# Kernel tuning notes

Measured on AMD Instinct MI355X. Metric: run time of the kernel, lower is better.

The kernel has to match this reference:

```python
import jax, jax.numpy as jnp
import numpy as np
import math

C_Z, C_HID, N_HEADS = 128, 32, 4
B, N = 1, 320
LN_EPS = 1e-5


def setup_inputs() -> dict:
    key = jax.random.key(0)
    ks = jax.random.split(key, 9)
    d = C_HID * N_HEADS  # 128
    glorot = math.sqrt(2.0 / (C_Z + d))
    return {
        "z": jax.random.normal(ks[0], (B, N, N, C_Z), jnp.float32),
        "mask_bias": jax.random.normal(ks[1], (B, N, 1, 1, N), jnp.float32),
        "edge_bias": jax.random.normal(ks[2], (B, 1, N_HEADS, N, N), jnp.float32),
        "wq": jax.random.normal(ks[3], (d, C_Z), jnp.float32) * glorot,
        "wk": jax.random.normal(ks[4], (d, C_Z), jnp.float32) * glorot,
        "wv": jax.random.normal(ks[5], (d, C_Z), jnp.float32) * glorot,
        "wg": jax.random.normal(ks[6], (d, C_Z), jnp.float32) * 0.02,
        "wo": jax.random.normal(ks[7], (C_Z, d), jnp.float32) * 0.02,
        "ln_w": jnp.ones((C_Z,), jnp.float32),
        "ln_b": jnp.zeros((C_Z,), jnp.float32),
    }


def reference(z, mask_bias, edge_bias, wq, wk, wv, wg, wo, ln_w, ln_b):
    # LayerNorm over c_z
    mu = jnp.mean(z, axis=-1, keepdims=True)
    var = jnp.mean(jnp.square(z - mu), axis=-1, keepdims=True)
    zn = (z - mu) * jax.lax.rsqrt(var + LN_EPS) * ln_w + ln_b  # [B,I,J,c_z]

    def proj(w):
        p = jnp.einsum("bijd,ed->bije", zn, w)  # [B,I,J,H*c]
        p = p.reshape(zn.shape[:-1] + (N_HEADS, C_HID))  # [B,I,J,H,c]
        return jnp.swapaxes(p, -3, -2)  # [B,I,H,J,c]

    q = proj(wq) / math.sqrt(C_HID)
    k = proj(wk)
    v = proj(wv)

    # scores: [B,I,H,Q,K] + mask_bias [B,I,1,1,K] + edge_bias [B,1,H,Q,K]
    scores = jnp.einsum("bihqc,bihkc->bihqk", q, k) + mask_bias + edge_bias
    a = jax.nn.softmax(scores, axis=-1)
    o = jnp.einsum("bihqk,bihkc->bihqc", a, v)  # [B,I,H,J,c]
    o = jnp.swapaxes(o, -3, -2)  # [B,I,J,H,c]

    g = jax.nn.sigmoid(jnp.einsum("bijd,ed->bije", zn, wg))
    g = g.reshape(zn.shape[:-1] + (N_HEADS, C_HID))
    o = o * g

    o = o.reshape(o.shape[:-2] + (N_HEADS * C_HID,))  # [B,I,J,H*c]
    return jnp.einsum("bije,de->bijd", o, wo)  # [B,I,J,c_z]
```

## Files before the change

### kernel.cpp

```cpp
#include <hip/hip_runtime.h>
#include <hip/hip_bf16.h>

#define NRES 320
#define CZ 128
#define NH 4
#define CH 32
#define DM 128
#define NPOS (NRES*NRES)
#define LN_EPS 1e-5f
#define QSCALE 0.17677669529663687f
#define LOG2E 1.4426950408889634f

using bf16 = __hip_bfloat16;
typedef __attribute__((ext_vector_type(8))) short short8;
typedef __attribute__((ext_vector_type(4))) float floatx4;

__device__ __forceinline__ float bflo(uint32_t u){ return __uint_as_float(u << 16); }
__device__ __forceinline__ float bfhi(uint32_t u){ return __uint_as_float(u & 0xffff0000u); }
__device__ __forceinline__ bf16 tob(float f){ return __float2bfloat16(f); }
__device__ __forceinline__ uint32_t cvtpk(float a, float b){
    uint32_t r;
    asm("v_cvt_pk_bf16_f32 %0, %1, %2" : "=v"(r) : "v"(a), "v"(b));
    return r;
}

__global__ __launch_bounds__(256)
void k_packall(const float* __restrict__ wq, const float* __restrict__ wk,
               const float* __restrict__ wv, const float* __restrict__ wg,
               const float* __restrict__ wo, const float* __restrict__ eb,
               const float* __restrict__ mb,
               bf16* __restrict__ Apkh, bf16* __restrict__ Apkl,
               bf16* __restrict__ B2h, bf16* __restrict__ B2l,
               bf16* __restrict__ ebpk, float* __restrict__ mbpk)
{
    const int idx = blockIdx.x * 256 + threadIdx.x;
    if (idx < 65536) {
        const int j = idx & 7, lane = (idx >> 3) & 63;
        const int ks = (idx >> 9) & 3, mf = (idx >> 11) & 3, wid = idx >> 13;
        const int e = wid*64 + mf*16 + (lane & 15);
        const int k = ks*32 + (lane >> 4)*8 + j;
        const float* w = (e >> 7) == 0 ? wq : (e >> 7) == 1 ? wk : (e >> 7) == 2 ? wv : wg;
        float wv_ = w[(e & 127)*CZ + k];
        if (e < 128) wv_ *= QSCALE * LOG2E;
        const bf16 hb = tob(wv_);
        Apkh[idx] = hb;
        Apkl[idx] = tob(wv_ - __bfloat162float(hb));
    } else if (idx < 81920) {
        const int id = idx - 65536;
        const int j = id & 7, lane = (id >> 3) & 63;
        const int nr = (id >> 9) & 3, ks = (id >> 11) & 3, wn = id >> 13;
        const int n = wn*64 + nr*16 + (lane & 15);
        const int k = ks*32 + ((lane >> 4) << 3) + j;
        const float wv_ = wo[n*DM + k];
        const bf16 hb = tob(wv_);
        B2h[id] = hb;
        B2l[id] = tob(wv_ - __bfloat162float(hb));
    } else if (idx < 491520) {
        const int id = idx - 81920;
        const int e = id & 7;
        const int lane = (id >> 3) & 63;
        const int f = (id >> 9) % 20;
        const int t = (id / 10240) % 10;
        const int h = id / 102400;
        const int q = f*16 + (lane & 15);
        const int k = t*32 + (e >> 2)*16 + (lane >> 4)*4 + (e & 3);
        ebpk[id] = tob(eb[((size_t)h*NRES + q)*NRES + k] * LOG2E);
    } else {
        const int id = idx - 491520;
        mbpk[id] = mb[id] * LOG2E;
    }
}

__global__ __launch_bounds__(512, 3)
void k_lnproj(const float* __restrict__ z, const float* __restrict__ ln_w,
              const float* __restrict__ ln_b, const bf16* __restrict__ Apkh,
              const bf16* __restrict__ Apkl,
              bf16* __restrict__ qws, bf16* __restrict__ kws,
              bf16* __restrict__ vtws, bf16* __restrict__ gows)
{
    __shared__ __align__(16) char Bsh[16 * 1040];
    __shared__ __align__(16) char Bsl[16 * 1040];
    const int tid = threadIdx.x;
    const int p0 = blockIdx.x * 64;
    const int lane = tid & 63, wid = tid >> 6;
    const int l15 = lane & 15, g = lane >> 4;

    {
        const int r = tid >> 3, t = tid & 7, c0 = t*16;
        const float* zp = z + (size_t)(p0 + r)*CZ + c0;
        float v[16];
        {
            float4 t0 = *(const float4*)(zp + 0);
            float4 t1 = *(const float4*)(zp + 4);
            float4 t2 = *(const float4*)(zp + 8);
            float4 t3 = *(const float4*)(zp + 12);
            v[0]=t0.x; v[1]=t0.y; v[2]=t0.z; v[3]=t0.w;
            v[4]=t1.x; v[5]=t1.y; v[6]=t1.z; v[7]=t1.w;
            v[8]=t2.x; v[9]=t2.y; v[10]=t2.z; v[11]=t2.w;
            v[12]=t3.x; v[13]=t3.y; v[14]=t3.z; v[15]=t3.w;
        }
        float s = 0.f, s2 = 0.f;
        #pragma unroll
        for (int c = 0; c < 16; ++c) { s += v[c]; s2 = fmaf(v[c], v[c], s2); }
        s  += __shfl_xor(s, 1);  s  += __shfl_xor(s, 2);  s  += __shfl_xor(s, 4);
        s2 += __shfl_xor(s2, 1); s2 += __shfl_xor(s2, 2); s2 += __shfl_xor(s2, 4);
        const float mu = s * 0.0078125f;
        const float rs = rsqrtf(s2 * 0.0078125f - mu*mu + LN_EPS);
        float vn[16];
        #pragma unroll
        for (int c = 0; c < 16; ++c)
            vn[c] = (v[c] - mu) * rs * ln_w[c0 + c] + ln_b[c0 + c];
        uint32_t hd[8], ld[8];
        #pragma unroll
        for (int c2 = 0; c2 < 8; ++c2) {
            hd[c2] = cvtpk(vn[2*c2], vn[2*c2+1]);
            ld[c2] = cvtpk(vn[2*c2]   - bflo(hd[c2]),
                           vn[2*c2+1] - bfhi(hd[c2]));
        }
        *(uint4*)(Bsh + (2*t    )*1040 + r*16) = make_uint4(hd[0], hd[1], hd[2], hd[3]);
        *(uint4*)(Bsh + (2*t + 1)*1040 + r*16) = make_uint4(hd[4], hd[5], hd[6], hd[7]);
        *(uint4*)(Bsl + (2*t    )*1040 + r*16) = make_uint4(ld[0], ld[1], ld[2], ld[3]);
        *(uint4*)(Bsl + (2*t + 1)*1040 + r*16) = make_uint4(ld[4], ld[5], ld[6], ld[7]);
    }
    __syncthreads();

    floatx4 acc[4][4];
    #pragma unroll
    for (int mf = 0; mf < 4; ++mf)
        #pragma unroll
        for (int nf = 0; nf < 4; ++nf)
            acc[mf][nf] = (floatx4){0.f, 0.f, 0.f, 0.f};

    const uint4* aph = (const uint4*)Apkh;
    const uint4* apl = (const uint4*)Apkl;
    #pragma unroll
    for (int ks = 0; ks < 4; ++ks) {
        uint4 ahv[4], alv[4];
        #pragma unroll
        for (int mf = 0; mf < 4; ++mf) {
            ahv[mf] = aph[((wid*4 + mf)*4 + ks)*64 + lane];
            alv[mf] = apl[((wid*4 + mf)*4 + ks)*64 + lane];
        }
        #pragma unroll
        for (int nf = 0; nf < 4; ++nf) {
            const int off = (ks*4 + g)*1040 + (16*nf + l15)*16;
            const short8 bh = *(const short8*)(Bsh + off);
            const short8 bl = *(const short8*)(Bsl + off);
            #pragma unroll
            for (int mf = 0; mf < 4; ++mf) {
                const short8 ah = *(const short8*)&ahv[mf];
                const short8 al = *(const short8*)&alv[mf];
                acc[mf][nf] = __builtin_amdgcn_mfma_f32_16x16x32_bf16(ah, bh, acc[mf][nf], 0, 0, 0);
                acc[mf][nf] = __builtin_amdgcn_mfma_f32_16x16x32_bf16(al, bh, acc[mf][nf], 0, 0, 0);
                acc[mf][nf] = __builtin_amdgcn_mfma_f32_16x16x32_bf16(ah, bl, acc[mf][nf], 0, 0, 0);
            }
        }
    }

    const int i = p0 / NRES;
    const int j0 = p0 % NRES;
    #pragma unroll
    for (int mf = 0; mf < 4; ++mf) {
        const int e0 = wid*64 + mf*16 + 4*g;
        const int hh = (e0 >> 5) & 3, c0 = e0 & 31;
        #pragma unroll
        for (int nf = 0; nf < 4; ++nf) {
            const int jl = nf*16 + l15;
            const floatx4 a = acc[mf][nf];
            if (wid < 4) {
                uint2 dw;
                dw.x = cvtpk(a[0], a[1]);
                dw.y = cvtpk(a[2], a[3]);
                bf16* dst = (wid < 2) ? qws : kws;
                const size_t hidx = ((size_t)((i*NH + hh)*NRES) + (j0 + jl))*CH + c0;
                *(uint2*)(dst + hidx) = dw;
            } else if (wid < 6) {
                const size_t vbase = ((size_t)((i*NH + hh)*CH) + c0)*NRES + (j0 + jl);
                vtws[vbase         ] = tob(a[0]);
                vtws[vbase +   NRES] = tob(a[1]);
                vtws[vbase + 2*NRES] = tob(a[2]);
                vtws[vbase + 3*NRES] = tob(a[3]);
            } else {
                const float g0 = 1.f / (1.f + __expf(-a[0]));
                const float g1 = 1.f / (1.f + __expf(-a[1]));
                const float g2 = 1.f / (1.f + __expf(-a[2]));
                const float g3 = 1.f / (1.f + __expf(-a[3]));
                uint2 dw;
                dw.x = cvtpk(g0, g1);
                dw.y = cvtpk(g2, g3);
                *(uint2*)(gows + (size_t)(p0 + jl)*DM + (e0 & 127)) = dw;
            }
        }
    }
}

__global__ __launch_bounds__(320, 3)
void k_attn(const bf16* __restrict__ qws, const bf16* __restrict__ kws,
            const bf16* __restrict__ vtws, bf16* __restrict__ gows,
            const float* __restrict__ mbpk, const bf16* __restrict__ ebpk)
{
    __shared__ __align__(16) char psmem[5 * 64 * 80];
    const int i = blockIdx.x, h = blockIdx.y;
    const int tid = threadIdx.x;
    const int lane = tid & 63, w = tid >> 6;
    const int l15 = lane & 15, g = lane >> 4;
    const size_t slab = (size_t)(i*NH + h) * NRES * CH;
    char* psb = psmem + w*5120;

    const uint4* qg = (const uint4*)(qws + slab);
    const uint4* kg = (const uint4*)(kws + slab);
    const uint4* vg = (const uint4*)(vtws + slab);
    const float* mbr = mbpk + (size_t)i*NRES;
    const uint4* ebp = (const uint4*)ebpk;
    const int ebbase = h*12800 + w*256 + lane;

    const uint32_t onep = (l15 == 0) ? 0x3F803F80u : 0u;
    uint4 au = make_uint4(onep, onep, onep, onep);
    const short8 av2 = *(short8*)&au;

    short8 bq[4];
    #pragma unroll
    for (int nf = 0; nf < 4; ++nf) {
        uint4 t = qg[(64*w + 16*nf + l15)*4 + g];
        bq[nf] = *(short8*)&t;
    }
    uint4 kc0 = kg[(     l15)*4 + g];
    uint4 kc1 = kg[(16 + l15)*4 + g];
    uint4 ebc[4];
    #pragma unroll
    for (int nf = 0; nf < 4; ++nf) ebc[nf] = ebp[ebbase + nf*64];

    floatx4 o[2][4];
    floatx4 o2[4];
    #pragma unroll
    for (int nf = 0; nf < 4; ++nf) {
        o[0][nf] = (floatx4){0.f, 0.f, 0.f, 0.f};
        o[1][nf] = (floatx4){0.f, 0.f, 0.f, 0.f};
        o2[nf]   = (floatx4){0.f, 0.f, 0.f, 0.f};
    }
    float m[4] = {-1e30f, -1e30f, -1e30f, -1e30f};

    for (int t = 0; t < 10; ++t) {
        const int tn = (t < 9) ? t + 1 : 9;
        uint4 kn0 = kg[(32*tn +      l15)*4 + g];
        uint4 kn1 = kg[(32*tn + 16 + l15)*4 + g];
        uint4 ebn[4];
        #pragma unroll
        for (int nf = 0; nf < 4; ++nf) ebn[nf] = ebp[ebbase + tn*1280 + nf*64];
        uint4 av0u = vg[(     l15)*40 + 4*t + g];
        uint4 av1u = vg[(16 + l15)*40 + 4*t + g];
        float2 mbv[2][2];
        #pragma unroll
        for (int mi = 0; mi < 2; ++mi)
            #pragma unroll
            for (int rp = 0; rp < 2; ++rp)
                mbv[mi][rp] = *(const float2*)(mbr + 32*t + 16*mi + 4*g + 2*rp);

        const short8 ak0 = *(short8*)&kc0;
        const short8 ak1 = *(short8*)&kc1;
        floatx4 sa[2][4];
        __builtin_amdgcn_s_setprio(1);
        #pragma unroll
        for (int nf = 0; nf < 4; ++nf) {
            const uint4 E = ebc[nf];
            const floatx4 c0 = (floatx4){bflo(E.x), bfhi(E.x), bflo(E.y), bfhi(E.y)};
            const floatx4 c1 = (floatx4){bflo(E.z), bfhi(E.z), bflo(E.w), bfhi(E.w)};
            sa[0][nf] = __builtin_amdgcn_mfma_f32_16x16x32_bf16(ak0, bq[nf], c0, 0, 0, 0);
            sa[1][nf] = __builtin_amdgcn_mfma_f32_16x16x32_bf16(ak1, bq[nf], c1, 0, 0, 0);
        }
        __builtin_amdgcn_s_setprio(0);

        float sv[4][2][4];
        float lmax[4];
        #pragma unroll
        for (int nf = 0; nf < 4; ++nf) {
            sv[nf][0][0] = sa[0][nf][0] + mbv[0][0].x;
            sv[nf][0][1] = sa[0][nf][1] + mbv[0][0].y;
            sv[nf][0][2] = sa[0][nf][2] + mbv[0][1].x;
            sv[nf][0][3] = sa[0][nf][3] + mbv[0][1].y;
            sv[nf][1][0] = sa[1][nf][0] + mbv[1][0].x;
            sv[nf][1][1] = sa[1][nf][1] + mbv[1][0].y;
            sv[nf][1][2] = sa[1][nf][2] + mbv[1][1].x;
            sv[nf][1][3] = sa[1][nf][3] + mbv[1][1].y;
            const float a0 = fmaxf(fmaxf(sv[nf][0][0], sv[nf][0][1]), fmaxf(sv[nf][0][2], sv[nf][0][3]));
            const float a1 = fmaxf(fmaxf(sv[nf][1][0], sv[nf][1][1]), fmaxf(sv[nf][1][2], sv[nf][1][3]));
            lmax[nf] = fmaxf(a0, a1);
        }
        const float gm = fmaxf(fmaxf(lmax[0] - m[0], lmax[1] - m[1]),
                               fmaxf(lmax[2] - m[2], lmax[3] - m[3]));
        if (__any(gm > 12.0f)) {
            #pragma unroll
            for (int nf = 0; nf < 4; ++nf) {
                float pm = lmax[nf];
                pm = fmaxf(pm, __shfl_xor(pm, 16));
                pm = fmaxf(pm, __shfl_xor(pm, 32));
                const float mn = fmaxf(m[nf], pm);
                const float sc = exp2f(m[nf] - mn);
                #pragma unroll
                for (int ma = 0; ma < 2; ++ma)
                    #pragma unroll
                    for (int r = 0; r < 4; ++r)
                        o[ma][nf][r] *= sc;
                #pragma unroll
                for (int r = 0; r < 4; ++r)
                    o2[nf][r] *= sc;
                m[nf] = mn;
            }
        }
        #pragma unroll
        for (int nf = 0; nf < 4; ++nf) {
            const int qrow = 16*nf + l15;
            #pragma unroll
            for (int mi = 0; mi < 2; ++mi) {
                const float p0 = exp2f(sv[nf][mi][0] - m[nf]);
                const float p1 = exp2f(sv[nf][mi][1] - m[nf]);
                const float p2 = exp2f(sv[nf][mi][2] - m[nf]);
                const float p3 = exp2f(sv[nf][mi][3] - m[nf]);
                *(uint2*)(psb + qrow*80 + 32*mi + 8*g) =
                    make_uint2(cvtpk(p0, p1), cvtpk(p2, p3));
            }
        }
        const short8 av0 = *(short8*)&av0u;
        const short8 av1 = *(short8*)&av1u;
        __builtin_amdgcn_s_setprio(1);
        #pragma unroll
        for (int nf = 0; nf < 4; ++nf) {
            const short8 bp = *(const short8*)(psb + (16*nf + l15)*80 + 16*g);
            o[0][nf] = __builtin_amdgcn_mfma_f32_16x16x32_bf16(av0, bp, o[0][nf], 0, 0, 0);
            o[1][nf] = __builtin_amdgcn_mfma_f32_16x16x32_bf16(av1, bp, o[1][nf], 0, 0, 0);
            o2[nf]   = __builtin_amdgcn_mfma_f32_16x16x32_bf16(av2, bp, o2[nf],   0, 0, 0);
        }
        __builtin_amdgcn_s_setprio(0);
        kc0 = kn0; kc1 = kn1;
        #pragma unroll
        for (int nf = 0; nf < 4; ++nf) ebc[nf] = ebn[nf];
    }

    float linv[4];
    #pragma unroll
    for (int nf = 0; nf < 4; ++nf) {
        const float ls = __shfl(o2[nf][0], l15);
        linv[nf] = 1.f / ls;
    }
    uint32_t* gp = (uint32_t*)gows;
    #pragma unroll
    for (int nf = 0; nf < 4; ++nf) {
        const int jq = 64*w + 16*nf + l15;
        #pragma unroll
        for (int ma = 0; ma < 2; ++ma)
            #pragma unroll
            for (int rp = 0; rp < 2; ++rp) {
                const size_t idx = ((size_t)(i*NRES + jq))*64 + h*16 + 8*ma + 2*g + rp;
                const uint32_t u = gp[idx];
                const float v0 = o[ma][nf][2*rp    ] * linv[nf] * bflo(u);
                const float v1 = o[ma][nf][2*rp + 1] * linv[nf] * bfhi(u);
                gp[idx] = cvtpk(v0, v1);
            }
    }
}

__global__ __launch_bounds__(512)
void k_outproj(const bf16* __restrict__ gows, const bf16* __restrict__ B2h,
               const bf16* __restrict__ B2l, float* __restrict__ out)
{
    __shared__ __align__(16) char As[16 * 4112];
    const int tid = threadIdx.x;
    const int p0 = blockIdx.x * 256;
    const int lane = tid & 63, wid = tid >> 6;
    const int wm = wid >> 1, wn = wid & 1;

    short8 bh[4][4];
    {
        const uint4* bp = (const uint4*)B2h;
        #pragma unroll
        for (int ks = 0; ks < 4; ++ks)
            #pragma unroll
            for (int nr = 0; nr < 4; ++nr) {
                uint4 t = bp[(((wn*4 + ks)*4) + nr)*64 + lane];
                bh[ks][nr] = *(short8*)&t;
            }
    }

    {
        const uint4* src = (const uint4*)(gows + (size_t)p0 * DM);
        #pragma unroll
        for (int it = 0; it < 8; ++it) {
            const int t = tid + it*512;
            uint4 u = src[t];
            *(uint4*)(As + (t & 15)*4112 + (t >> 4)*16) = u;
        }
    }
    __syncthreads();

    floatx4 acc[4][4];
    #pragma unroll
    for (int m = 0; m < 4; ++m)
        #pragma unroll
        for (int n = 0; n < 4; ++n)
            acc[m][n] = (floatx4){0.f, 0.f, 0.f, 0.f};

    const uint4* bpl = (const uint4*)B2l;
    #pragma unroll
    for (int ks = 0; ks < 4; ++ks) {
        short8 a[4];
        #pragma unroll
        for (int m = 0; m < 4; ++m) {
            const int row = wm*64 + m*16 + (lane & 15);
            a[m] = *(const short8*)(As + (ks*4 + (lane >> 4))*4112 + row*16);
        }
        #pragma unroll
        for (int nr = 0; nr < 4; ++nr) {
            uint4 tl = bpl[(((wn*4 + ks)*4) + nr)*64 + lane];
            const short8 bl = *(short8*)&tl;
            #pragma unroll
            for (int m = 0; m < 4; ++m)
                acc[m][nr] = __builtin_amdgcn_mfma_f32_16x16x32_bf16(a[m], bh[ks][nr], acc[m][nr], 0, 0, 0);
            #pragma unroll
            for (int m = 0; m < 4; ++m)
                acc[m][nr] = __builtin_amdgcn_mfma_f32_16x16x32_bf16(a[m], bl, acc[m][nr], 0, 0, 0);
        }
    }

    #pragma unroll
    for (int m = 0; m < 4; ++m) {
        #pragma unroll
        for (int n = 0; n < 4; ++n) {
            const int d = wn*64 + n*16 + (lane & 15);
            #pragma unroll
            for (int r = 0; r < 4; ++r) {
                const int prow = p0 + wm*64 + m*16 + ((lane >> 4) << 2) + r;
                out[(size_t)prow*DM + d] = acc[m][n][r];
            }
        }
    }
}

extern "C" void kernel_launch(void* const* d_in, const int* in_sizes, int n_in,
                              void* d_out, int out_size, void* d_ws, size_t ws_size,
                              hipStream_t stream)
{
    const float* z   = (const float*)d_in[0];
    const float* mb  = (const float*)d_in[1];
    const float* eb  = (const float*)d_in[2];
    const float* wq  = (const float*)d_in[3];
    const float* wk  = (const float*)d_in[4];
    const float* wv  = (const float*)d_in[5];
    const float* wg  = (const float*)d_in[6];
    const float* wo  = (const float*)d_in[7];
    const float* lnw = (const float*)d_in[8];
    const float* lnb = (const float*)d_in[9];
    float* out = (float*)d_out;

    const size_t SEG = (size_t)NPOS * DM;
    bf16* qws  = (bf16*)d_ws;
    bf16* kws  = qws + SEG;
    bf16* vtws = kws + SEG;
    bf16* gows = vtws + SEG;
    bf16* Apkh = gows + SEG;
    bf16* Apkl = Apkh + 65536;
    bf16* B2h  = Apkl + 65536;
    bf16* B2l  = B2h + 16384;
    bf16* ebpk = B2l + 16384;
    float* mbpk = (float*)(ebpk + 409600);

    k_packall<<<2320, 256, 0, stream>>>(wq, wk, wv, wg, wo, eb, mb,
                                        Apkh, Apkl, B2h, B2l, ebpk, mbpk);
    k_lnproj<<<NPOS/64, 512, 0, stream>>>(z, lnw, lnb, Apkh, Apkl, qws, kws, vtws, gows);
    k_attn<<<dim3(NRES, NH), 320, 0, stream>>>(qws, kws, vtws, gows, mbpk, ebpk);
    k_outproj<<<NPOS/256, 512, 0, stream>>>(gows, B2h, B2l, out);
}
```

Before: 159.5 us.

## Software-pipeline QK scores one tile ahead of softmax and PV

Restructures the attention inner loop so the QK^T MFMAs for tile t+1 are issued after the PV MFMAs of tile t. K and edge-bias loads are prefetched two tiles ahead, with A/B double-buffered registers and a 2x manual unroll via a macro. The aim is to overlap score MFMAs with the softmax VALU work and to hide global-load latency. It raises register pressure, which could lower occupancy. The last iteration computes one redundant score tile.

Measured after the change: 252.8 us. 1.59x slower.

```diff
diff --git a/kernel.cpp b/kernel.cpp
--- a/kernel.cpp
+++ b/kernel.cpp
@@ -224,11 +224,6 @@
         uint4 t = qg[(64*w + 16*nf + l15)*4 + g];
         bq[nf] = *(short8*)&t;
     }
-    uint4 kc0 = kg[(     l15)*4 + g];
-    uint4 kc1 = kg[(16 + l15)*4 + g];
-    uint4 ebc[4];
-    #pragma unroll
-    for (int nf = 0; nf < 4; ++nf) ebc[nf] = ebp[ebbase + nf*64];
 
     floatx4 o[2][4];
     floatx4 o2[4];
@@ -239,102 +234,148 @@
         o2[nf]   = (floatx4){0.f, 0.f, 0.f, 0.f};
     }
     float m[4] = {-1e30f, -1e30f, -1e30f, -1e30f};
-
-    for (int t = 0; t < 10; ++t) {
-        const int tn = (t < 9) ? t + 1 : 9;
-        uint4 kn0 = kg[(32*tn +      l15)*4 + g];
-        uint4 kn1 = kg[(32*tn + 16 + l15)*4 + g];
-        uint4 ebn[4];
-        #pragma unroll
-        for (int nf = 0; nf < 4; ++nf) ebn[nf] = ebp[ebbase + tn*1280 + nf*64];
-        uint4 av0u = vg[(     l15)*40 + 4*t + g];
-        uint4 av1u = vg[(16 + l15)*40 + 4*t + g];
-        float2 mbv[2][2];
-        #pragma unroll
-        for (int mi = 0; mi < 2; ++mi)
-            #pragma unroll
-            for (int rp = 0; rp < 2; ++rp)
-                mbv[mi][rp] = *(const float2*)(mbr + 32*t + 16*mi + 4*g + 2*rp);
-
-        const short8 ak0 = *(short8*)&kc0;
-        const short8 ak1 = *(short8*)&kc1;
-        floatx4 sa[2][4];
-        __builtin_amdgcn_s_setprio(1);
+    floatx4 sa[2][4];
+
+    uint4 kA0, kA1, kB0, kB1;
+    uint4 ebA[4], ebB[4];
+    uint4 vA0, vA1, vB0, vB1;
+    float2 mbA[2][2], mbB[2][2];
+
+    kA0 = kg[(     l15)*4 + g];
+    kA1 = kg[(16 + l15)*4 + g];
+    #pragma unroll
+    for (int nf = 0; nf < 4; ++nf) ebA[nf] = ebp[ebbase + nf*64];
+    {
+        const short8 a0 = *(short8*)&kA0;
+        const short8 a1 = *(short8*)&kA1;
         #pragma unroll
         for (int nf = 0; nf < 4; ++nf) {
-            const uint4 E = ebc[nf];
+            const uint4 E = ebA[nf];
             const floatx4 c0 = (floatx4){bflo(E.x), bfhi(E.x), bflo(E.y), bfhi(E.y)};
             const floatx4 c1 = (floatx4){bflo(E.z), bfhi(E.z), bflo(E.w), bfhi(E.w)};
-            sa[0][nf] = __builtin_amdgcn_mfma_f32_16x16x32_bf16(ak0, bq[nf], c0, 0, 0, 0);
-            sa[1][nf] = __builtin_amdgcn_mfma_f32_16x16x32_bf16(ak1, bq[nf], c1, 0, 0, 0);
-        }
-        __builtin_amdgcn_s_setprio(0);
-
-        float sv[4][2][4];
-        float lmax[4];
-        #pragma unroll
-        for (int nf = 0; nf < 4; ++nf) {
-            sv[nf][0][0] = sa[0][nf][0] + mbv[0][0].x;
-            sv[nf][0][1] = sa[0][nf][1] + mbv[0][0].y;
-            sv[nf][0][2] = sa[0][nf][2] + mbv[0][1].x;
-            sv[nf][0][3] = sa[0][nf][3] + mbv[0][1].y;
-            sv[nf][1][0] = sa[1][nf][0] + mbv[1][0].x;
-            sv[nf][1][1] = sa[1][nf][1] + mbv[1][0].y;
-            sv[nf][1][2] = sa[1][nf][2] + mbv[1][1].x;
-            sv[nf][1][3] = sa[1][nf][3] + mbv[1][1].y;
-            const float a0 = fmaxf(fmaxf(sv[nf][0][0], sv[nf][0][1]), fmaxf(sv[nf][0][2], sv[nf][0][3]));
-            const float a1 = fmaxf(fmaxf(sv[nf][1][0], sv[nf][1][1]), fmaxf(sv[nf][1][2], sv[nf][1][3]));
-            lmax[nf] = fmaxf(a0, a1);
-        }
-        const float gm = fmaxf(fmaxf(lmax[0] - m[0], lmax[1] - m[1]),
-                               fmaxf(lmax[2] - m[2], lmax[3] - m[3]));
-        if (__any(gm > 12.0f)) {
-            #pragma unroll
-            for (int nf = 0; nf < 4; ++nf) {
-                float pm = lmax[nf];
-                pm = fmaxf(pm, __shfl_xor(pm, 16));
-                pm = fmaxf(pm, __shfl_xor(pm, 32));
-                const float mn = fmaxf(m[nf], pm);
-                const float sc = exp2f(m[nf] - mn);
-                #pragma unroll
-                for (int ma = 0; ma < 2; ++ma)
-                    #pragma unroll
-                    for (int r = 0; r < 4; ++r)
-                        o[ma][nf][r] *= sc;
-                #pragma unroll
-                for (int r = 0; r < 4; ++r)
-                    o2[nf][r] *= sc;
-                m[nf] = mn;
-            }
-        }
-        #pragma unroll
-        for (int nf = 0; nf < 4; ++nf) {
-            const int qrow = 16*nf + l15;
-            #pragma unroll
-            for (int mi = 0; mi < 2; ++mi) {
-                const float p0 = exp2f(sv[nf][mi][0] - m[nf]);
-                const float p1 = exp2f(sv[nf][mi][1] - m[nf]);
-                const float p2 = exp2f(sv[nf][mi][2] - m[nf]);
-                const float p3 = exp2f(sv[nf][mi][3] - m[nf]);
-                *(uint2*)(psb + qrow*80 + 32*mi + 8*g) =
-                    make_uint2(cvtpk(p0, p1), cvtpk(p2, p3));
-            }
-        }
-        const short8 av0 = *(short8*)&av0u;
-        const short8 av1 = *(short8*)&av1u;
-        __builtin_amdgcn_s_setprio(1);
-        #pragma unroll
-        for (int nf = 0; nf < 4; ++nf) {
-            const short8 bp = *(const short8*)(psb + (16*nf + l15)*80 + 16*g);
-            o[0][nf] = __builtin_amdgcn_mfma_f32_16x16x32_bf16(av0, bp, o[0][nf], 0, 0, 0);
-            o[1][nf] = __builtin_amdgcn_mfma_f32_16x16x32_bf16(av1, bp, o[1][nf], 0, 0, 0);
-            o2[nf]   = __builtin_amdgcn_mfma_f32_16x16x32_bf16(av2, bp, o2[nf],   0, 0, 0);
-        }
-        __builtin_amdgcn_s_setprio(0);
-        kc0 = kn0; kc1 = kn1;
-        #pragma unroll
-        for (int nf = 0; nf < 4; ++nf) ebc[nf] = ebn[nf];
-    }
+            sa[0][nf] = __builtin_amdgcn_mfma_f32_16x16x32_bf16(a0, bq[nf], c0, 0, 0, 0);
+            sa[1][nf] = __builtin_amdgcn_mfma_f32_16x16x32_bf16(a1, bq[nf], c1, 0, 0, 0);
+        }
+    }
+    kB0 = kg[(32 +      l15)*4 + g];
+    kB1 = kg[(32 + 16 + l15)*4 + g];
+    #pragma unroll
+    for (int nf = 0; nf < 4; ++nf) ebB[nf] = ebp[ebbase + 1280 + nf*64];
+    vA0 = vg[(     l15)*40 + g];
+    vA1 = vg[(16 + l15)*40 + g];
+    #pragma unroll
+    for (int mi = 0; mi < 2; ++mi)
+        #pragma unroll
+        for (int rp = 0; rp < 2; ++rp)
+            mbA[mi][rp] = *(const float2*)(mbr + 16*mi + 4*g + 2*rp);
+
+#define ATTN_BODY(T, KU0, KU1, EBU, VU0, VU1, MBU, KL0, KL1, EBL, VL0, VL1, MBL)   \
+    {                                                                              \
+        const int tn1 = ((T) < 9) ? (T) + 1 : 9;                                   \
+        const int tn2 = ((T) < 8) ? (T) + 2 : 9;                                   \
+                         \
+        KL0 = kg[(32*tn2 +      l15)*4 + g];                                       \
+        KL1 = kg[(32*tn2 + 16 + l15)*4 + g];                                       \
+        _Pragma("unroll")                                                          \
+        for (int nf = 0; nf < 4; ++nf) EBL[nf] = ebp[ebbase + tn2*1280 + nf*64];   \
+        VL0 = vg[(     l15)*40 + 4*tn1 + g];                                       \
+        VL1 = vg[(16 + l15)*40 + 4*tn1 + g];                                       \
+        _Pragma("unroll")                                                          \
+        for (int mi = 0; mi < 2; ++mi)                                             \
+            _Pragma("unroll")                                                      \
+            for (int rp = 0; rp < 2; ++rp)                                         \
+                MBL[mi][rp] = *(const float2*)(mbr + 32*tn1 + 16*mi + 4*g + 2*rp); \
+                           \
+        float sv[4][2][4];                                                         \
+        float lmax[4];                                                             \
+        _Pragma("unroll")                                                          \
+        for (int nf = 0; nf < 4; ++nf) {                                           \
+            sv[nf][0][0] = sa[0][nf][0] + MBU[0][0].x;                             \
+            sv[nf][0][1] = sa[0][nf][1] + MBU[0][0].y;                             \
+            sv[nf][0][2] = sa[0][nf][2] + MBU[0][1].x;                             \
+            sv[nf][0][3] = sa[0][nf][3] + MBU[0][1].y;                             \
+            sv[nf][1][0] = sa[1][nf][0] + MBU[1][0].x;                             \
+            sv[nf][1][1] = sa[1][nf][1] + MBU[1][0].y;                             \
+            sv[nf][1][2] = sa[1][nf][2] + MBU[1][1].x;                             \
+            sv[nf][1][3] = sa[1][nf][3] + MBU[1][1].y;                             \
+            const float a0 = fmaxf(fmaxf(sv[nf][0][0], sv[nf][0][1]),              \
+                                   fmaxf(sv[nf][0][2], sv[nf][0][3]));             \
+            const float a1 = fmaxf(fmaxf(sv[nf][1][0], sv[nf][1][1]),              \
+                                   fmaxf(sv[nf][1][2], sv[nf][1][3]));             \
+            lmax[nf] = fmaxf(a0, a1);                                              \
+        }                                                                          \
+        const float gm = fmaxf(fmaxf(lmax[0] - m[0], lmax[1] - m[1]),              \
+                               fmaxf(lmax[2] - m[2], lmax[3] - m[3]));             \
+        if (__any(gm > 12.0f)) {                                                   \
+            _Pragma("unroll")                                                      \
+            for (int nf = 0; nf < 4; ++nf) {                                       \
+                float pm = lmax[nf];                                               \
+                pm = fmaxf(pm, __shfl_xor(pm, 16));                                \
+                pm = fmaxf(pm, __shfl_xor(pm, 32));                                \
+                const float mn = fmaxf(m[nf], pm);                                 \
+                const float sc = exp2f(m[nf] - mn);                                \
+                _Pragma("unroll")                                                  \
+                for (int ma = 0; ma < 2; ++ma)                                     \
+                    _Pragma("unroll")                                              \
+                    for (int r = 0; r < 4; ++r)                                    \
+                        o[ma][nf][r] *= sc;                                        \
+                _Pragma("unroll")                                                  \
+                for (int r = 0; r < 4; ++r)                                        \
+                    o2[nf][r] *= sc;                                               \
+                m[nf] = mn;                                                        \
+            }                                                                      \
+        }                                                                          \
+        _Pragma("unroll")                                                          \
+        for (int nf = 0; nf < 4; ++nf) {                                           \
+            const int qrow = 16*nf + l15;                                          \
+            _Pragma("unroll")                                                      \
+            for (int mi = 0; mi < 2; ++mi) {                                       \
+                const float p0 = exp2f(sv[nf][mi][0] - m[nf]);                     \
+                const float p1 = exp2f(sv[nf][mi][1] - m[nf]);                     \
+                const float p2 = exp2f(sv[nf][mi][2] - m[nf]);                     \
+                const float p3 = exp2f(sv[nf][mi][3] - m[nf]);                     \
+                *(uint2*)(psb + qrow*80 + 32*mi + 8*g) =                           \
+                    make_uint2(cvtpk(p0, p1), cvtpk(p2, p3));                      \
+            }                                                                      \
+        }                                                                          \
+                                                                       \
+        {                                                                          \
+            const short8 av0 = *(short8*)&VU0;                                     \
+            const short8 av1 = *(short8*)&VU1;                                     \
+            __builtin_amdgcn_s_setprio(1);                                         \
+            _Pragma("unroll")                                                      \
+            for (int nf = 0; nf < 4; ++nf) {                                       \
+                const short8 bp = *(const short8*)(psb + (16*nf + l15)*80 + 16*g); \
+                o[0][nf] = __builtin_amdgcn_mfma_f32_16x16x32_bf16(av0, bp, o[0][nf], 0, 0, 0); \
+                o[1][nf] = __builtin_amdgcn_mfma_f32_16x16x32_bf16(av1, bp, o[1][nf], 0, 0, 0); \
+                o2[nf]   = __builtin_amdgcn_mfma_f32_16x16x32_bf16(av2, bp, o2[nf],   0, 0, 0); \
+            }                                                                      \
+            __builtin_amdgcn_s_setprio(0);                                         \
+        }                                                                          \
+        \
+        {                                                                          \
+            const short8 a0 = *(short8*)&KU0;                                      \
+            const short8 a1 = *(short8*)&KU1;                                      \
+            __builtin_amdgcn_s_setprio(1);                                         \
+            _Pragma("unroll")                                                      \
+            for (int nf = 0; nf < 4; ++nf) {                                       \
+                const uint4 E = EBU[nf];                                           \
+                const floatx4 c0 = (floatx4){bflo(E.x), bfhi(E.x), bflo(E.y), bfhi(E.y)}; \
+                const floatx4 c1 = (floatx4){bflo(E.z), bfhi(E.z), bflo(E.w), bfhi(E.w)}; \
+                sa[0][nf] = __builtin_amdgcn_mfma_f32_16x16x32_bf16(a0, bq[nf], c0, 0, 0, 0); \
+                sa[1][nf] = __builtin_amdgcn_mfma_f32_16x16x32_bf16(a1, bq[nf], c1, 0, 0, 0); \
+            }                                                                      \
+            __builtin_amdgcn_s_setprio(0);                                         \
+        }                                                                          \
+    }
+
+    for (int tp = 0; tp < 5; ++tp) {
+        ATTN_BODY(2*tp,     kB0, kB1, ebB, vA0, vA1, mbA,
+                            kA0, kA1, ebA, vB0, vB1, mbB)
+        ATTN_BODY(2*tp + 1, kA0, kA1, ebA, vB0, vB1, mbB,
+                            kB0, kB1, ebB, vA0, vA1, mbA)
+    }
+#undef ATTN_BODY
 
     float linv[4];
     #pragma unroll
```
